# Optimization experiments

Hardware: AMD Instinct MI355X
Metric: run time of the kernel (lower is better)

The kernel has to match this reference:

```python
import jax, jax.numpy as jnp
import numpy as np

K, S, P, NQ, NREPS = 3, 1, 1, 9, 2  # kernel, stride, pad, num_qubits, num_qreps


def _extract_patches(x, k, s):
    # x: (b, c, H, W) -> (b, c, ho, wo, k*k), patch elems in (kh, kw) row-major order
    b, c, H, W = x.shape
    ho = (H - k) // s + 1
    wo = (W - k) // s + 1
    cols = [x[:, :, i:i + (ho - 1) * s + 1:s, j:j + (wo - 1) * s + 1:s]
            for i in range(k) for j in range(k)]
    return jnp.stack(cols, axis=-1), ho, wo


def _cnot(state, c, t):
    # state: (N, 2, ..., 2); CNOT with control wire c, target wire t (wire q -> axis q+1)
    s0, s1 = jnp.split(state, 2, axis=c + 1)
    return jnp.concatenate([s0, jnp.flip(s1, axis=t + 1)], axis=c + 1)


def _simulate(angles, weights):
    # AngleEmbedding(RX) + BasicEntanglerLayers(RZ, CNOT ring) + expval(PauliY_i)
    # angles: (N, n) float; weights: (L, n) float -> (N, n) float expvals
    N, n = angles.shape
    half = 0.5 * angles
    # RX(theta)|0> = cos(t/2)|0> - i sin(t/2)|1>  (product state)
    vecs = jnp.stack([jnp.cos(half).astype(jnp.complex64),
                      -1j * jnp.sin(half)], axis=-1)  # (N, n, 2)
    state = vecs[:, 0]
    for q in range(1, n):
        state = state[..., None] * vecs[:, q].reshape((N,) + (1,) * q + (2,))
    # state: (N, 2, ..., 2), wire 0 = axis 1 (most significant)
    for l in range(weights.shape[0]):
        # RZ layer = single diagonal of shape (2,)*n, shared across patches
        pv = jnp.stack([jnp.exp(-0.5j * weights[l]),
                        jnp.exp(0.5j * weights[l])], axis=-1).astype(jnp.complex64)  # (n,2)
        diag = pv[0]
        for q in range(1, n):
            diag = diag[..., None] * pv[q].reshape((1,) * q + (2,))
        state = state * diag
        # CNOT ring (i -> i+1 mod n), as in BasicEntanglerLayers for n > 2
        for i in range(n):
            state = _cnot(state, i, (i + 1) % n)
    # <Y_i> = 2 * Im( sum conj(psi_{qi=0}) * psi_{qi=1} )
    exps = []
    for i in range(n):
        a, bdim = 1 << i, 1 << (n - 1 - i)
        r = state.reshape(N, a, 2, bdim)
        z = jnp.sum(jnp.conj(r[:, :, 0, :]) * r[:, :, 1, :], axis=(1, 2))
        exps.append(2.0 * z.imag)
    return jnp.stack(exps, axis=1)  # (N, n) float32


def setup_inputs() -> dict:
    key = jax.random.key(0)
    k1, k2 = jax.random.split(key)
    x = jax.random.uniform(k1, (16, 1, 28, 28), dtype=jnp.float32)
    weights = jax.random.uniform(k2, (NREPS, NQ), dtype=jnp.float32,
                                 minval=0.0, maxval=2.0 * np.pi)
    return {"x": x, "weights": weights}


def reference(x, weights):
    b = x.shape[0]
    xp = jnp.pad(x, ((0, 0), (0, 0), (P, P), (P, P)))
    patches, ho, wo = _extract_patches(xp, K, S)  # (b, 1, ho, wo, k*k)
    flat = patches.reshape(-1, NQ)                # (b*ho*wo, 9)  (c == 1)
    qout = _simulate(flat, weights)               # (b*ho*wo, 9)
    qout = qout.reshape(b, ho, wo, NQ)
    return qout.transpose(0, 3, 1, 2)             # (b, 9, ho, wo)
```

## Files before the change

kernel.cpp:

```cpp
#include <hip/hip_runtime.h>
#include <math.h>

#define NQ 9
#define NREPS 2
#define NB 512
#define NSIMS (16*28*28)

__host__ __device__ constexpr int csigma(int b) {
    for (int c = NQ - 1; c >= 0; --c) {
        const int t  = (c + 1) % NQ;
        const int pc = NQ - 1 - c;
        const int pt = NQ - 1 - t;
        b ^= ((b >> pc) & 1) << pt;
    }
    return b;
}
__host__ __device__ constexpr int csig2(int b) { return csigma(csigma(b)); }

constexpr int VB_[6] = { csig2(1<<0), csig2(1<<1), csig2(1<<2),
                         csig2(1<<3), csig2(1<<4), csig2(1<<5) };
constexpr int VR_[8] = { csig2(0<<6), csig2(1<<6), csig2(2<<6), csig2(3<<6),
                         csig2(4<<6), csig2(5<<6), csig2(6<<6), csig2(7<<6) };

__device__ float2 g_T[NB];

__global__ void quanv_setup(const float* __restrict__ w) {
    const int b = threadIdx.x;
    if (b >= NB) return;
    float th = 0.f;
    int cur = b;
    #pragma unroll
    for (int l = NREPS - 1; l >= 0; --l) {
        cur = csigma(cur);
        #pragma unroll
        for (int q = 0; q < NQ; ++q) {
            const float wq = 0.5f * w[l * NQ + q];
            th += ((cur >> (NQ - 1 - q)) & 1) ? wq : -wq;
        }
    }
    th -= 1.5707963267948966f * (float)__popc((unsigned)cur);
    g_T[b] = make_float2(cosf(th), sinf(th));
}

template<int CTRL>
__device__ __forceinline__ float dppmov(float x) {
    return __int_as_float(__builtin_amdgcn_update_dpp(
        0, __float_as_int(x), CTRL, 0xF, 0xF, true));
}
template<int OFF>
__device__ __forceinline__ float swzx(float x) {
    return __int_as_float(__builtin_amdgcn_ds_swizzle(__float_as_int(x), OFF));
}
template<int P>
__device__ __forceinline__ float lane_xor(float x) {
    if constexpr (P == 0) return dppmov<0xB1>(x);
    else if constexpr (P == 1) return dppmov<0x4E>(x);
    else if constexpr (P == 2) return swzx<0x101F>(x);
    else if constexpr (P == 3) return dppmov<0x128>(x);
    else if constexpr (P == 4) return swzx<0x401F>(x);
    else return __shfl_xor(x, 32, 64);
}
__device__ __forceinline__ float wave_reduce(float v) {
    v += dppmov<0x111>(v);
    v += dppmov<0x112>(v);
    v += dppmov<0x114>(v);
    v += dppmov<0x118>(v);
    v += dppmov<0x142>(v);
    v += dppmov<0x143>(v);
    return v;
}

__global__ __launch_bounds__(256) void quanv_main(
    const float* __restrict__ x,
    float* __restrict__ out)
{
    const int tid  = blockIdx.x * blockDim.x + threadIdx.x;
    const int lane = threadIdx.x & 63;
    const int sim  = tid >> 6;
    const int ox  = sim % 28;
    const int oy  = (sim / 28) % 28;
    const int img = sim / 784;

    float cq[NQ], sq[NQ];
    #pragma unroll
    for (int q = 0; q < NQ; ++q) {
        const int ky = q / 3, kx = q % 3;
        const int y  = oy + ky - 1;
        const int xx = ox + kx - 1;
        float a = 0.f;
        if (y >= 0 && y < 28 && xx >= 0 && xx < 28)
            a = x[img * 784 + y * 28 + xx];
        __sincosf(0.5f * a, &sq[q], &cq[q]);
    }

    const int VL = ((lane & 1)  ? VB_[0] : 0) ^ ((lane & 2)  ? VB_[1] : 0)
                 ^ ((lane & 4)  ? VB_[2] : 0) ^ ((lane & 8)  ? VB_[3] : 0)
                 ^ ((lane & 16) ? VB_[4] : 0) ^ ((lane & 32) ? VB_[5] : 0);

    float P0[NQ], P1[NQ];
    #pragma unroll
    for (int q = 0; q < NQ; ++q) {
        const bool bit = (VL >> (NQ - 1 - q)) & 1;
        P0[q] = bit ? sq[q] : cq[q];
        P1[q] = bit ? cq[q] : sq[q];
    }

    float fre[8], fim[8];
    #pragma unroll
    for (int r = 0; r < 8; ++r) {
        float m = ((VR_[r] >> (NQ - 1)) & 1) ? P1[0] : P0[0];
        #pragma unroll
        for (int q = 1; q < NQ; ++q)
            m *= ((VR_[r] >> (NQ - 1 - q)) & 1) ? P1[q] : P0[q];
        const float2 T = g_T[(r << 6) | lane];
        fre[r] = m * T.x;
        fim[r] = m * T.y;
    }

    float e[NQ];
#define EXP_QUBIT(i, P)                                            \
    {                                                              \
        const float sign = ((lane >> (P)) & 1) ? -1.f : 1.f;       \
        float acc = 0.f;                                           \
        _Pragma("unroll")                                          \
        for (int r = 0; r < 8; ++r) {                              \
            const float gre = lane_xor<P>(fre[r]);                 \
            const float gim = lane_xor<P>(fim[r]);                 \
            acc += fre[r] * gim - fim[r] * gre;                    \
        }                                                          \
        e[i] = sign * acc;                                         \
    }
    EXP_QUBIT(8, 0)
    EXP_QUBIT(7, 1)
    EXP_QUBIT(6, 2)
    EXP_QUBIT(5, 3)
    EXP_QUBIT(4, 4)
    EXP_QUBIT(3, 5)
#undef EXP_QUBIT

    #pragma unroll
    for (int i = 0; i < 3; ++i) {
        const int rb = (NQ - 1 - i) - 6;
        float acc = 0.f;
        #pragma unroll
        for (int r = 0; r < 8; ++r) {
            if (!((r >> rb) & 1)) {
                const int r1 = r | (1 << rb);
                acc += fre[r] * fim[r1] - fim[r] * fre[r1];
            }
        }
        e[i] = 2.f * acc;
    }

    #pragma unroll
    for (int i = 0; i < NQ; ++i)
        e[i] = wave_reduce(e[i]);

    if (lane == 63) {
        float* o = out + img * (NQ * 784) + oy * 28 + ox;
        #pragma unroll
        for (int i = 0; i < NQ; ++i)
            o[i * 784] = e[i];
    }
}

extern "C" void kernel_launch(void* const* d_in, const int* in_sizes, int n_in,
                              void* d_out, int out_size, void* d_ws, size_t ws_size,
                              hipStream_t stream) {
    const float* x = (const float*)d_in[0];
    const float* w = (const float*)d_in[1];
    float* out = (float*)d_out;
    (void)d_ws; (void)ws_size; (void)in_sizes; (void)n_in; (void)out_size;

    quanv_setup<<<1, NB, 0, stream>>>(w);
    quanv_main<<<NSIMS / 4, 256, 0, stream>>>(x, out);
}
```

Before: 67.81 us.

## Replace statevector simulation with per-block Walsh-Hadamard coefficient polynomial evaluation

Drops the wave-per-patch statevector simulation. Each block now derives, from the weights, a Walsh-Hadamard-transformed coefficient table in shared memory, and each thread evaluates every qubit's expectation as a multilinear polynomial in cos/sin of the patch angles. The setup kernel is folded into the main kernel, so every block recomputes the phase table and the transforms. This removes the cross-lane shuffles and reductions and handles one patch per thread instead of one per wave, at the cost of redundant per-block setup work and several __syncthreads barriers.

```diff
diff --git a/kernel.cpp b/kernel.cpp
--- a/kernel.cpp
+++ b/kernel.cpp
@@ -17,151 +17,151 @@
 }
 __host__ __device__ constexpr int csig2(int b) { return csigma(csigma(b)); }
 
-constexpr int VB_[6] = { csig2(1<<0), csig2(1<<1), csig2(1<<2),
-                         csig2(1<<3), csig2(1<<4), csig2(1<<5) };
-constexpr int VR_[8] = { csig2(0<<6), csig2(1<<6), csig2(2<<6), csig2(3<<6),
-                         csig2(4<<6), csig2(5<<6), csig2(6<<6), csig2(7<<6) };
-
-__device__ float2 g_T[NB];
-
-__global__ void quanv_setup(const float* __restrict__ w) {
-    const int b = threadIdx.x;
-    if (b >= NB) return;
-    float th = 0.f;
-    int cur = b;
-    #pragma unroll
-    for (int l = NREPS - 1; l >= 0; --l) {
-        cur = csigma(cur);
-        #pragma unroll
-        for (int q = 0; q < NQ; ++q) {
-            const float wq = 0.5f * w[l * NQ + q];
-            th += ((cur >> (NQ - 1 - q)) & 1) ? wq : -wq;
-        }
-    }
-    th -= 1.5707963267948966f * (float)__popc((unsigned)cur);
-    g_T[b] = make_float2(cosf(th), sinf(th));
+__host__ __device__ constexpr int PIOF(int i)  { return NQ - 1 - i; }
+__host__ __device__ constexpr int VMASK(int i) { return csig2(1 << PIOF(i)); }
+__host__ __device__ constexpr int SCOMP(int i) { return (~VMASK(i)) & ((1 << NQ) - 1); }
+__host__ __device__ constexpr int NV(int i)    { int m = SCOMP(i), c = 0; while (m) { c += m & 1; m >>= 1; } return c; }
+__host__ __device__ constexpr int CBASE(int i) { int s = 0; for (int k = 0; k < i; ++k) s += 1 << NV(k); return s; }
+__host__ __device__ constexpr int POSI(int i, int t) {
+    int m = SCOMP(i), p = 0;
+    while (true) { if (m & 1) { if (t == 0) return p; --t; } m >>= 1; ++p; }
 }
 
-template<int CTRL>
-__device__ __forceinline__ float dppmov(float x) {
-    return __int_as_float(__builtin_amdgcn_update_dpp(
-        0, __float_as_int(x), CTRL, 0xF, 0xF, true));
-}
-template<int OFF>
-__device__ __forceinline__ float swzx(float x) {
-    return __int_as_float(__builtin_amdgcn_ds_swizzle(__float_as_int(x), OFF));
-}
-template<int P>
-__device__ __forceinline__ float lane_xor(float x) {
-    if constexpr (P == 0) return dppmov<0xB1>(x);
-    else if constexpr (P == 1) return dppmov<0x4E>(x);
-    else if constexpr (P == 2) return swzx<0x101F>(x);
-    else if constexpr (P == 3) return dppmov<0x128>(x);
-    else if constexpr (P == 4) return swzx<0x401F>(x);
-    else return __shfl_xor(x, 32, 64);
-}
-__device__ __forceinline__ float wave_reduce(float v) {
-    v += dppmov<0x111>(v);
-    v += dppmov<0x112>(v);
-    v += dppmov<0x114>(v);
-    v += dppmov<0x118>(v);
-    v += dppmov<0x142>(v);
-    v += dppmov<0x143>(v);
-    return v;
+__device__ const int d_COL[NQ] = {
+    csig2(1 << 0), csig2(1 << 1), csig2(1 << 2), csig2(1 << 3), csig2(1 << 4),
+    csig2(1 << 5), csig2(1 << 6), csig2(1 << 7), csig2(1 << 8)
+};
+
+template<int L>
+__device__ __forceinline__ float heval(const float* __restrict__ cf, const float* vx) {
+    if constexpr (L == 2) {
+        const float4 g = *reinterpret_cast<const float4*>(cf);
+        return (g.x + vx[0] * g.y) + vx[1] * (g.z + vx[0] * g.w);
+    } else {
+        return heval<L - 1>(cf, vx) + vx[L - 1] * heval<L - 1>(cf + (1 << (L - 1)), vx);
+    }
 }
 
-__global__ __launch_bounds__(256) void quanv_main(
+template<int I>
+__device__ __forceinline__ float qubit_eval(const float* __restrict__ coefI,
+                                            const float* ca, const float* sa) {
+    constexpr int V = NV(I);
+    float vx[7];
+    if constexpr (V > 0) vx[0] = ca[NQ - 1 - POSI(I, 0)];
+    if constexpr (V > 1) vx[1] = ca[NQ - 1 - POSI(I, 1)];
+    if constexpr (V > 2) vx[2] = ca[NQ - 1 - POSI(I, 2)];
+    if constexpr (V > 3) vx[3] = ca[NQ - 1 - POSI(I, 3)];
+    if constexpr (V > 4) vx[4] = ca[NQ - 1 - POSI(I, 4)];
+    if constexpr (V > 5) vx[5] = ca[NQ - 1 - POSI(I, 5)];
+    if constexpr (V > 6) vx[6] = ca[NQ - 1 - POSI(I, 6)];
+    const float g = heval<V>(coefI, vx);
+    float sp = 1.f;
+    if constexpr ((VMASK(I) & (1 << 0)) != 0) sp *= sa[8];
+    if constexpr ((VMASK(I) & (1 << 1)) != 0) sp *= sa[7];
+    if constexpr ((VMASK(I) & (1 << 2)) != 0) sp *= sa[6];
+    if constexpr ((VMASK(I) & (1 << 3)) != 0) sp *= sa[5];
+    if constexpr ((VMASK(I) & (1 << 4)) != 0) sp *= sa[4];
+    if constexpr ((VMASK(I) & (1 << 5)) != 0) sp *= sa[3];
+    if constexpr ((VMASK(I) & (1 << 6)) != 0) sp *= sa[2];
+    if constexpr ((VMASK(I) & (1 << 7)) != 0) sp *= sa[1];
+    if constexpr ((VMASK(I) & (1 << 8)) != 0) sp *= sa[0];
+    return sp * g;
+}
+
+__global__ __launch_bounds__(256) void quanv_fused(
     const float* __restrict__ x,
+    const float* __restrict__ w,
     float* __restrict__ out)
 {
-    const int tid  = blockIdx.x * blockDim.x + threadIdx.x;
-    const int lane = threadIdx.x & 63;
-    const int sim  = tid >> 6;
+    __shared__ float sTc[NB], sTs[NB];
+    __shared__ float sD[NQ][256];
+    __shared__ __align__(16) float sCoef[1024];
+    const int tid = threadIdx.x;
+
+    for (int b = tid; b < NB; b += 256) {
+        float th = 0.f;
+        int cur = b;
+        #pragma unroll
+        for (int l = NREPS - 1; l >= 0; --l) {
+            cur = csigma(cur);
+            #pragma unroll
+            for (int q = 0; q < NQ; ++q) {
+                const float wq = 0.5f * w[l * NQ + q];
+                th += ((cur >> (NQ - 1 - q)) & 1) ? wq : -wq;
+            }
+        }
+        th -= 1.5707963267948966f * (float)__popc((unsigned)cur);
+        float s, c;
+        sincosf(th, &s, &c);
+        sTc[b] = c; sTs[b] = s;
+    }
+    __syncthreads();
+
+    for (int idx = tid; idx < NQ * 256; idx += 256) {
+        const int i  = idx >> 8, y = idx & 255;
+        const int Pi = NQ - 1 - i;
+        const int b  = ((y >> Pi) << (Pi + 1)) | (y & ((1 << Pi) - 1));
+        const int b2 = b | (1 << Pi);
+        sD[i][y] = sTs[b2] * sTc[b] - sTc[b2] * sTs[b];
+    }
+    __syncthreads();
+
+    for (int s = 0; s < 8; ++s) {
+        for (int idx = tid; idx < NQ * 128; idx += 256) {
+            const int i  = idx >> 7, k = idx & 127;
+            const int y0 = ((k >> s) << (s + 1)) | (k & ((1 << s) - 1));
+            const int y1 = y0 | (1 << s);
+            const float a = sD[i][y0], bb = sD[i][y1];
+            sD[i][y0] = a + bb;
+            sD[i][y1] = a - bb;
+        }
+        __syncthreads();
+    }
+
+    for (int idx = tid; idx < 1024; idx += 256) {
+        int i, u;
+        if (idx < 896)      { i = idx >> 7; u = idx & 127; }
+        else if (idx < 960) { i = 7; u = idx - 896; }
+        else                { i = 8; u = idx - 960; }
+        const int Pi = NQ - 1 - i;
+        int sc = (~d_COL[Pi]) & ((1 << NQ) - 1);
+        int J = 0, uu = u;
+        while (sc) { const int low = sc & (-sc); if (uu & 1) J |= low; sc &= sc - 1; uu >>= 1; }
+        int MJ = 0;
+        #pragma unroll
+        for (int k = 0; k < NQ; ++k) MJ |= (__popc((unsigned)(d_COL[k] & J)) & 1) << k;
+        const int w8 = ((MJ >> (Pi + 1)) << Pi) | (MJ & ((1 << Pi) - 1));
+        sCoef[idx] = sD[i][w8] * (1.0f / 256.0f);
+    }
+    __syncthreads();
+
+    const int sim = blockIdx.x * 256 + tid;
     const int ox  = sim % 28;
-    const int oy  = (sim / 28) % 28;
-    const int img = sim / 784;
+    const int t1  = sim / 28;
+    const int oy  = t1 % 28;
+    const int img = t1 / 28;
 
-    float cq[NQ], sq[NQ];
+    float ca[NQ], sa[NQ];
     #pragma unroll
     for (int q = 0; q < NQ; ++q) {
         const int ky = q / 3, kx = q % 3;
-        const int y  = oy + ky - 1;
-        const int xx = ox + kx - 1;
+        const int yy = oy + ky - 1, xx = ox + kx - 1;
         float a = 0.f;
-        if (y >= 0 && y < 28 && xx >= 0 && xx < 28)
-            a = x[img * 784 + y * 28 + xx];
-        __sincosf(0.5f * a, &sq[q], &cq[q]);
+        if (yy >= 0 && yy < 28 && xx >= 0 && xx < 28)
+            a = x[img * 784 + yy * 28 + xx];
+        __sincosf(a, &sa[q], &ca[q]);
     }
 
-    const int VL = ((lane & 1)  ? VB_[0] : 0) ^ ((lane & 2)  ? VB_[1] : 0)
-                 ^ ((lane & 4)  ? VB_[2] : 0) ^ ((lane & 8)  ? VB_[3] : 0)
-                 ^ ((lane & 16) ? VB_[4] : 0) ^ ((lane & 32) ? VB_[5] : 0);
-
-    float P0[NQ], P1[NQ];
-    #pragma unroll
-    for (int q = 0; q < NQ; ++q) {
-        const bool bit = (VL >> (NQ - 1 - q)) & 1;
-        P0[q] = bit ? sq[q] : cq[q];
-        P1[q] = bit ? cq[q] : sq[q];
-    }
-
-    float fre[8], fim[8];
-    #pragma unroll
-    for (int r = 0; r < 8; ++r) {
-        float m = ((VR_[r] >> (NQ - 1)) & 1) ? P1[0] : P0[0];
-        #pragma unroll
-        for (int q = 1; q < NQ; ++q)
-            m *= ((VR_[r] >> (NQ - 1 - q)) & 1) ? P1[q] : P0[q];
-        const float2 T = g_T[(r << 6) | lane];
-        fre[r] = m * T.x;
-        fim[r] = m * T.y;
-    }
-
-    float e[NQ];
-#define EXP_QUBIT(i, P)                                            \
-    {                                                              \
-        const float sign = ((lane >> (P)) & 1) ? -1.f : 1.f;       \
-        float acc = 0.f;                                           \
-        _Pragma("unroll")                                          \
-        for (int r = 0; r < 8; ++r) {                              \
-            const float gre = lane_xor<P>(fre[r]);                 \
-            const float gim = lane_xor<P>(fim[r]);                 \
-            acc += fre[r] * gim - fim[r] * gre;                    \
-        }                                                          \
-        e[i] = sign * acc;                                         \
-    }
-    EXP_QUBIT(8, 0)
-    EXP_QUBIT(7, 1)
-    EXP_QUBIT(6, 2)
-    EXP_QUBIT(5, 3)
-    EXP_QUBIT(4, 4)
-    EXP_QUBIT(3, 5)
-#undef EXP_QUBIT
-
-    #pragma unroll
-    for (int i = 0; i < 3; ++i) {
-        const int rb = (NQ - 1 - i) - 6;
-        float acc = 0.f;
-        #pragma unroll
-        for (int r = 0; r < 8; ++r) {
-            if (!((r >> rb) & 1)) {
-                const int r1 = r | (1 << rb);
-                acc += fre[r] * fim[r1] - fim[r] * fre[r1];
-            }
-        }
-        e[i] = 2.f * acc;
-    }
-
-    #pragma unroll
-    for (int i = 0; i < NQ; ++i)
-        e[i] = wave_reduce(e[i]);
-
-    if (lane == 63) {
-        float* o = out + img * (NQ * 784) + oy * 28 + ox;
-        #pragma unroll
-        for (int i = 0; i < NQ; ++i)
-            o[i * 784] = e[i];
-    }
+    float* o = out + img * (NQ * 784) + oy * 28 + ox;
+    o[0 * 784] = qubit_eval<0>(sCoef + CBASE(0), ca, sa);
+    o[1 * 784] = qubit_eval<1>(sCoef + CBASE(1), ca, sa);
+    o[2 * 784] = qubit_eval<2>(sCoef + CBASE(2), ca, sa);
+    o[3 * 784] = qubit_eval<3>(sCoef + CBASE(3), ca, sa);
+    o[4 * 784] = qubit_eval<4>(sCoef + CBASE(4), ca, sa);
+    o[5 * 784] = qubit_eval<5>(sCoef + CBASE(5), ca, sa);
+    o[6 * 784] = qubit_eval<6>(sCoef + CBASE(6), ca, sa);
+    o[7 * 784] = qubit_eval<7>(sCoef + CBASE(7), ca, sa);
+    o[8 * 784] = qubit_eval<8>(sCoef + CBASE(8), ca, sa);
 }
 
 extern "C" void kernel_launch(void* const* d_in, const int* in_sizes, int n_in,
@@ -172,6 +172,5 @@
     float* out = (float*)d_out;
     (void)d_ws; (void)ws_size; (void)in_sizes; (void)n_in; (void)out_size;
 
-    quanv_setup<<<1, NB, 0, stream>>>(w);
-    quanv_main<<<NSIMS / 4, 256, 0, stream>>>(x, out);
+    quanv_fused<<<NSIMS / 256, 256, 0, stream>>>(x, w, out);
 }
```

Result: slower. 78.18 us (+15.3%).
